# Performance work log

Measured on AMD Instinct MI355X. Metric: run time of the kernel, lower is better.

## Reference

```python
import math
import jax, jax.numpy as jnp
import numpy as np
from jax.scipy.special import xlogy, gammaln

HEADS = 8
DIM_KEY = 64
NUM_REL_POS_FEATURES = 192


def get_positional_embed(n, feature_size):
    # distances: [-n+1, ..., n-1], length 2n-1
    dist = jnp.arange(-n + 1, n)
    adist = jnp.abs(dist).astype(jnp.float32)[:, None]  # (2n-1, 1)
    num_basis = feature_size // 6  # 3 feature fns * 2 (sign-augmented)
    seq_len = n
    # exponential half-life features
    max_range = math.log(seq_len) / math.log(2.0)
    half_life = 2.0 ** jnp.linspace(3.0, max_range, num_basis)  # min_half_life=3.0
    feat_exp = jnp.exp(-math.log(2.0) / half_life[None, :] * adist)
    # central mask features
    center_widths = 2.0 ** jnp.arange(1, num_basis + 1) - 1.0
    feat_cm = (center_widths[None, :] > adist).astype(jnp.float32)
    # gamma pdf features
    stddev = seq_len / (2 * num_basis)
    start_mean = seq_len / num_basis
    mean = jnp.linspace(start_mean, float(seq_len), num_basis)[None, :]
    concentration = (mean / stddev) ** 2
    rate = mean / (stddev ** 2)
    log_unnorm = xlogy(concentration - 1.0, adist) - rate * adist
    log_norm = gammaln(concentration) - concentration * jnp.log(rate)
    prob = jnp.exp(log_unnorm - log_norm) + 1e-8
    feat_gamma = prob / jnp.max(prob, axis=-1, keepdims=True)
    emb = jnp.concatenate([feat_exp, feat_cm, feat_gamma], axis=-1)  # (2n-1, fs/2)
    sign = jnp.sign(dist).astype(jnp.float32)[:, None]
    return jnp.concatenate([emb, sign * emb], axis=-1)  # (2n-1, fs)


def relative_shift(x):
    # x: (b, h, n, 2n-1) -> (b, h, n, n) Transformer-XL shift
    b, h, t1, t2 = x.shape
    x = jnp.pad(x, ((0, 0), (0, 0), (0, 0), (1, 0)))  # (b,h,t1,t2+1)
    x = x.reshape(b, h, t2 + 1, t1)[:, :, 1:, :].reshape(b, h, t1, t2)
    return x[..., : (t2 + 2) // 2]


def setup_inputs() -> dict:
    key = jax.random.key(0)
    ks = jax.random.split(key, 8)
    dim = 1536
    b, n = 2, 1536
    hdk = HEADS * DIM_KEY  # 512
    hdv = HEADS * 192      # 1536
    s = 0.02
    return {
        'x': jax.random.normal(ks[0], (b, n, dim), jnp.float32),
        'Wq': jax.random.normal(ks[1], (hdk, dim), jnp.float32) * s,
        'Wk': jax.random.normal(ks[2], (hdk, dim), jnp.float32) * s,
        'Wv': jax.random.normal(ks[3], (hdv, dim), jnp.float32) * s,
        'Wrel': jax.random.normal(ks[4], (hdk, NUM_REL_POS_FEATURES), jnp.float32) * s,
        'Wout': jax.random.normal(ks[5], (dim, hdv), jnp.float32) * s,
        'b_out': jnp.zeros((dim,), jnp.float32),
        'rel_content_bias': jax.random.normal(ks[6], (1, HEADS, 1, DIM_KEY), jnp.float32),
        'rel_pos_bias': jax.random.normal(ks[7], (1, HEADS, 1, DIM_KEY), jnp.float32),
    }


def reference(x, Wq, Wk, Wv, Wrel, Wout, b_out, rel_content_bias, rel_pos_bias):
    b, n, dim = x.shape
    h = HEADS
    scale = DIM_KEY ** -0.5

    def split_heads(t):  # (b, n, h*d) -> (b, h, n, d)
        return t.reshape(b, n, h, -1).transpose(0, 2, 1, 3)

    q = split_heads(jnp.einsum('bnd,fd->bnf', x, Wq)) * scale
    k = split_heads(jnp.einsum('bnd,fd->bnf', x, Wk))
    v = split_heads(jnp.einsum('bnd,fd->bnf', x, Wv))

    content_logits = jnp.einsum('bhid,bhjd->bhij', q + rel_content_bias, k)

    positions = get_positional_embed(n, NUM_REL_POS_FEATURES)  # (2n-1, fs)
    rel_k = jnp.einsum('jf,ef->je', positions, Wrel).reshape(2 * n - 1, h, DIM_KEY)
    rel_k = rel_k.transpose(1, 0, 2)  # (h, 2n-1, dk)
    rel_logits = jnp.einsum('bhid,hjd->bhij', q + rel_pos_bias, rel_k)
    rel_logits = relative_shift(rel_logits)  # (b, h, n, n)

    attn = jax.nn.softmax(content_logits + rel_logits, axis=-1)
    out = jnp.einsum('bhij,bhjd->bhid', attn, v)
    out = out.transpose(0, 2, 1, 3).reshape(b, n, -1)  # (b, n, h*dv)
    return jnp.einsum('bnf,df->bnd', out, Wout) + b_out
```

## Files before the change

kernel.cpp:

```cpp
#include <hip/hip_runtime.h>
#include <cmath>

typedef unsigned short u16;
typedef unsigned int u32;
typedef short frag8 __attribute__((ext_vector_type(8)));
typedef float f32x4 __attribute__((ext_vector_type(4)));

#define DEVINL __device__ __forceinline__

DEVINL float bf2f(u16 v) { return __uint_as_float(((u32)v) << 16); }
DEVINL u16 f2bf(float f) {
    u32 u = __float_as_uint(f);
    u32 r = (u + 0x7fffu + ((u >> 16) & 1u)) >> 16;
    return (u16)r;
}
DEVINL u32 pack2(float a, float b) { return (u32)f2bf(a) | ((u32)f2bf(b) << 16); }
DEVINL void async_copy16(const u16* g, u16* l) {
    __builtin_amdgcn_global_load_lds((const __attribute__((address_space(1))) u32*)g,
                                     (__attribute__((address_space(3))) u32*)l, 16, 0, 0);
}
DEVINL f32x4 mfma_bf16(frag8 a, frag8 b, f32x4 c) {
    return __builtin_amdgcn_mfma_f32_16x16x32_bf16(a, b, c, 0, 0, 0);
}

__global__ __launch_bounds__(256) void convert_kernel(
        const float* __restrict__ s0, const float* __restrict__ s1,
        const float* __restrict__ s2, const float* __restrict__ s3,
        const float* __restrict__ s4, u16* __restrict__ dst) {
    const int c0 = 589824, c1 = 98304, c2 = 98304, c3 = 294912;
    const int total = 1376256;
    for (int c = blockIdx.x * blockDim.x + threadIdx.x; c < total;
         c += gridDim.x * blockDim.x) {
        const float* src; int off;
        if (c < c0) { src = s0; off = c; }
        else if (c < c0 + c1) { src = s1; off = c - c0; }
        else if (c < c0 + c1 + c2) { src = s2; off = c - c0 - c1; }
        else if (c < c0 + c1 + c2 + c3) { src = s3; off = c - c0 - c1 - c2; }
        else { src = s4; off = c - c0 - c1 - c2 - c3; }
        float4 a = ((const float4*)src)[off * 2];
        float4 b = ((const float4*)src)[off * 2 + 1];
        uint4 o;
        o.x = pack2(a.x, a.y); o.y = pack2(a.z, a.w);
        o.z = pack2(b.x, b.y); o.w = pack2(b.z, b.w);
        ((uint4*)dst)[c] = o;
    }
}

DEVINL double lgamma_stirling(double z) {
    double zi = 1.0 / z, zi2 = zi * zi;
    return (z - 0.5) * log(z) - z + 0.91893853320467274178
         + zi * (1.0 / 12.0) - zi * zi2 * (1.0 / 360.0) + zi * zi2 * zi2 * (1.0 / 1260.0);
}

__global__ __launch_bounds__(256) void embed_relk_kernel(const float* __restrict__ Wrel,
                                                         u16* __restrict__ relk) {
    __shared__ float pos[16][192];
    __shared__ float inv_hl[32], cwid[32], cm1[32], rateS[32];
    __shared__ double lognS[32];
    __shared__ float gmax[16];
    int t = threadIdx.x;
    int u0b = blockIdx.x * 16;

    if (t < 32) {
        double step = (10.584962500721156 - 3.0) / 31.0;
        double hl = exp2(3.0 + t * step);
        inv_hl[t] = (float)(1.0 / hl);
        cwid[t] = exp2f((float)(t + 1)) - 1.0f;
        double mean = 48.0 * (t + 1);
        double conc = (mean / 24.0) * (mean / 24.0);
        double rate = mean / 576.0;
        cm1[t] = (float)(conc - 1.0);
        rateS[t] = (float)rate;
        lognS[t] = lgamma_stirling(conc) - conc * log(rate);
    }
    __syncthreads();

    for (int idx = t; idx < 512; idx += 256) {
        int ul = idx >> 5, bs = idx & 31;
        int dist = u0b + ul - 1535;
        float ad = fabsf((float)dist);
        pos[ul][bs] = exp2f(-ad * inv_hl[bs]);
        pos[ul][32 + bs] = (cwid[bs] > ad) ? 1.0f : 0.0f;
        double prob = 0.0;
        if (dist != 0) {
            double adD = (double)ad;
            prob = exp((double)cm1[bs] * log(adD) - (double)rateS[bs] * adD - lognS[bs]);
        }
        pos[ul][64 + bs] = (float)(prob + 1e-8);
    }
    __syncthreads();
    if (t < 16) {
        float g = 0.f;
        #pragma unroll
        for (int bsx = 0; bsx < 32; bsx++) g = fmaxf(g, pos[t][64 + bsx]);
        gmax[t] = g;
    }
    __syncthreads();
    for (int idx = t; idx < 16 * 96; idx += 256) {
        int ul = idx / 96, f = idx - ul * 96;
        float v = pos[ul][f];
        if (f >= 64) { v = v / gmax[ul]; pos[ul][f] = v; }
        int dist = u0b + ul - 1535;
        float sg = (dist > 0) ? 1.f : ((dist < 0) ? -1.f : 0.f);
        pos[ul][96 + f] = sg * v;
    }
    __syncthreads();

    int e0 = t * 2;
    const float* w0 = Wrel + e0 * 192;
    const float* w1 = w0 + 192;
    float a0[16], a1[16];
    #pragma unroll
    for (int ul = 0; ul < 16; ul++) { a0[ul] = 0.f; a1[ul] = 0.f; }
    for (int f = 0; f < 192; f++) {
        float wa = w0[f], wb = w1[f];
        #pragma unroll
        for (int ul = 0; ul < 16; ul++) {
            float p = pos[ul][f];
            a0[ul] = fmaf(p, wa, a0[ul]);
            a1[ul] = fmaf(p, wb, a1[ul]);
        }
    }
    int h0 = e0 >> 6, d0 = e0 & 63;
    int h1 = (e0 + 1) >> 6, d1 = (e0 + 1) & 63;
    for (int ul = 0; ul < 16; ul++) {
        int u = u0b + ul;
        relk[(h0 * 3072 + u) * 64 + d0] = f2bf(a0[ul]);
        relk[(h1 * 3072 + u) * 64 + d1] = f2bf(a1[ul]);
    }
}

DEVINL void gemm128_mainloop(const u16* __restrict__ A, const u16* __restrict__ B,
                             int K, f32x4 acc[4][4], u16* As, u16* Bs) {
    int tid = threadIdx.x;
    int lane = tid & 63, wave = tid >> 6;
    int wm = (wave >> 1) * 64, wn = (wave & 1) * 64;
    int fm = lane & 15, fq = lane >> 4;
    for (int k0 = 0; k0 < K; k0 += 32) {
        #pragma unroll
        for (int p = 0; p < 2; p++) {
            int e = (p * 256 + tid) * 8;
            int r = e >> 5, c = e & 31;
            async_copy16(A + r * K + k0 + c, As + e);
            async_copy16(B + r * K + k0 + c, Bs + e);
        }
        __syncthreads();
        frag8 af[4], bfr[4];
        #pragma unroll
        for (int mi = 0; mi < 4; mi++) af[mi] = *(const frag8*)&As[(wm + 16 * mi + fm) * 32 + fq * 8];
        #pragma unroll
        for (int ni = 0; ni < 4; ni++) bfr[ni] = *(const frag8*)&Bs[(wn + 16 * ni + fm) * 32 + fq * 8];
        #pragma unroll
        for (int mi = 0; mi < 4; mi++)
            #pragma unroll
            for (int ni = 0; ni < 4; ni++)
                acc[mi][ni] = mfma_bf16(af[mi], bfr[ni], acc[mi][ni]);
        __syncthreads();
    }
}

__global__ __launch_bounds__(256) void gemm_qkv_kernel(
        const u16* __restrict__ X, const u16* __restrict__ Wq, const u16* __restrict__ Wk,
        const u16* __restrict__ Wv, const float* __restrict__ cbias, const float* __restrict__ pbias,
        u16* __restrict__ qc, u16* __restrict__ qp, u16* __restrict__ kws, u16* __restrict__ vt) {
    __shared__ __align__(16) u16 As[128 * 32];
    __shared__ __align__(16) u16 Bs[128 * 32];
    int m0 = blockIdx.x * 128, n0 = blockIdx.y * 128;
    const u16* Bp; int brow;
    if (n0 < 512)       { Bp = Wq; brow = n0; }
    else if (n0 < 1024) { Bp = Wk; brow = n0 - 512; }
    else                { Bp = Wv; brow = n0 - 1024; }
    f32x4 acc[4][4];
    #pragma unroll
    for (int i = 0; i < 4; i++)
        #pragma unroll
        for (int j = 0; j < 4; j++) acc[i][j] = (f32x4){0.f, 0.f, 0.f, 0.f};
    gemm128_mainloop(X + m0 * 1536, Bp + brow * 1536, 1536, acc, As, Bs);

    int tid = threadIdx.x, lane = tid & 63, wave = tid >> 6;
    int wm = (wave >> 1) * 64, wn = (wave & 1) * 64, fm = lane & 15, fq = lane >> 4;
    #pragma unroll
    for (int mi = 0; mi < 4; mi++) {
        #pragma unroll
        for (int ni = 0; ni < 4; ni++) {
            int col = n0 + wn + 16 * ni + fm;
            int rbase = m0 + wm + 16 * mi + fq * 4;
            #pragma unroll
            for (int reg = 0; reg < 4; reg++) {
                int row = rbase + reg;
                float v = acc[mi][ni][reg];
                int b = row >= 1536 ? 1 : 0;
                int i = row - b * 1536;
                if (n0 < 512) {
                    float qv = v * 0.125f;
                    int idx = ((b * 8 + (col >> 6)) * 1536 + i) * 64 + (col & 63);
                    qc[idx] = f2bf(qv + cbias[col]);
                    qp[idx] = f2bf(qv + pbias[col]);
                } else if (n0 < 1024) {
                    int c2 = col - 512;
                    kws[((b * 8 + (c2 >> 6)) * 1536 + i) * 64 + (c2 & 63)] = f2bf(v);
                } else {
                    int c2 = col - 1024;
                    int hh = c2 / 192, dd = c2 - hh * 192;
                    vt[((b * 8 + hh) * 192 + dd) * 1536 + i] = f2bf(v);
                }
            }
        }
    }
}

#define SP 68
#define RP 100

__global__ __launch_bounds__(256, 3) void attn_kernel(
        const u16* __restrict__ qc, const u16* __restrict__ qp, const u16* __restrict__ kws,
        const u16* __restrict__ vt, const u16* __restrict__ relk, u16* __restrict__ ao) {
    __shared__ __align__(16) float S_lds[32 * SP];
    __shared__ __align__(16) float R_lds[32 * RP];
    __shared__ __align__(16) u16 P_lds[32 * 64];
    __shared__ float mstate[32], lstate[32], alpha_lds[32];

    const int n = 1536;
    int bh = blockIdx.y, b = bh >> 3, h = bh & 7;
    int i0 = blockIdx.x * 32;
    const u16* qcP = qc + bh * n * 64;
    const u16* qpP = qp + bh * n * 64;

    int tid = threadIdx.x, lane = tid & 63, w = tid >> 6, fm = lane & 15, fq = lane >> 4;
    int sw = fm & 7;
    if (tid < 32) { mstate[tid] = __int_as_float(0xff800000); lstate[tid] = 0.f; }

    frag8 aqc[2][2], aqp[2][2];
    #pragma unroll
    for (int mi = 0; mi < 2; mi++)
        #pragma unroll
        for (int ks = 0; ks < 2; ks++) {
            int off = (i0 + 16 * mi + fm) * 64 + ks * 32 + fq * 8;
            aqc[mi][ks] = *(const frag8*)(qcP + off);
            aqp[mi][ks] = *(const frag8*)(qpP + off);
        }

    f32x4 acc_o[2][3];
    #pragma unroll
    for (int mi = 0; mi < 2; mi++)
        #pragma unroll
        for (int dj = 0; dj < 3; dj++) acc_o[mi][dj] = (f32x4){0.f, 0.f, 0.f, 0.f};

    int uis[3], rmis[3];
    #pragma unroll
    for (int tt = 0; tt < 3; tt++) {
        int tv = w + tt * 4;
        rmis[tt] = (tv >= 6) ? 1 : 0;
        uis[tt] = tv - rmis[tt] * 6;
    }

    const u16* kIt  = kws + bh * n * 64 + (16 * w + fm) * 64 + fq * 8;
    const u16* vIt  = vt + bh * 192 * n + (48 * w + fm) * 1536 + fq * 8;
    const u16* rk0  = relk + h * 3072 * 64 + (1504 - i0 + fm) * 64 + fq * 8 + uis[0] * 1024;
    const u16* rk1  = relk + h * 3072 * 64 + (1504 - i0 + fm) * 64 + fq * 8 + uis[1] * 1024;
    const u16* rk2  = relk + h * 3072 * 64 + (1504 - i0 + fm) * 64 + fq * 8 + uis[2] * 1024;

    for (int jt = 0; jt < 24; jt++) {
        frag8 fk[2], fr0[2], fr1[2], fr2[2];
        fk[0]  = *(const frag8*)(kIt);
        fk[1]  = *(const frag8*)(kIt + 32);
        fr0[0] = *(const frag8*)(rk0);
        fr0[1] = *(const frag8*)(rk0 + 32);
        fr1[0] = *(const frag8*)(rk1);
        fr1[1] = *(const frag8*)(rk1 + 32);
        fr2[0] = *(const frag8*)(rk2);
        fr2[1] = *(const frag8*)(rk2 + 32);
        kIt += 4096; rk0 += 4096; rk1 += 4096; rk2 += 4096;

        f32x4 acc_s[2];
        acc_s[0] = (f32x4){0.f, 0.f, 0.f, 0.f};
        acc_s[1] = (f32x4){0.f, 0.f, 0.f, 0.f};
        #pragma unroll
        for (int ks = 0; ks < 2; ks++) {
            acc_s[0] = mfma_bf16(aqc[0][ks], fk[ks], acc_s[0]);
            acc_s[1] = mfma_bf16(aqc[1][ks], fk[ks], acc_s[1]);
        }
        f32x4 acc_r[3];
        #pragma unroll
        for (int tt = 0; tt < 3; tt++) acc_r[tt] = (f32x4){0.f, 0.f, 0.f, 0.f};
        #pragma unroll
        for (int ks = 0; ks < 2; ks++) {
            acc_r[0] = mfma_bf16(aqp[rmis[0]][ks], fr0[ks], acc_r[0]);
            acc_r[1] = mfma_bf16(aqp[rmis[1]][ks], fr1[ks], acc_r[1]);
            acc_r[2] = mfma_bf16(aqp[rmis[2]][ks], fr2[ks], acc_r[2]);
        }

        #pragma unroll
        for (int mi = 0; mi < 2; mi++)
            #pragma unroll
            for (int reg = 0; reg < 4; reg++)
                S_lds[(16 * mi + fq * 4 + reg) * SP + 16 * w + fm] = acc_s[mi][reg];
        #pragma unroll
        for (int tt = 0; tt < 3; tt++)
            #pragma unroll
            for (int reg = 0; reg < 4; reg++)
                R_lds[(16 * rmis[tt] + fq * 4 + reg) * RP + 16 * uis[tt] + fm] = acc_r[tt][reg];
        __syncthreads();

        frag8 fv[3][2];
        #pragma unroll
        for (int dj = 0; dj < 3; dj++)
            #pragma unroll
            for (int ks = 0; ks < 2; ks++)
                fv[dj][ks] = *(const frag8*)(vIt + dj * 24576 + ks * 32);
        vIt += 64;

        int li = tid >> 3, c0 = (tid & 7) * 8;
        float sv[8];
        {
            float4 sa = *(const float4*)(S_lds + li * SP + c0);
            float4 sb = *(const float4*)(S_lds + li * SP + c0 + 4);
            sv[0] = sa.x; sv[1] = sa.y; sv[2] = sa.z; sv[3] = sa.w;
            sv[4] = sb.x; sv[5] = sb.y; sv[6] = sb.z; sv[7] = sb.w;
        }
        const float* rrow = R_lds + li * RP + c0 - li + 31;
        float mx = __int_as_float(0xff800000);
        #pragma unroll
        for (int e = 0; e < 8; e++) {
            sv[e] += rrow[e];
            mx = fmaxf(mx, sv[e]);
        }
        mx = fmaxf(mx, __shfl_xor(mx, 1));
        mx = fmaxf(mx, __shfl_xor(mx, 2));
        mx = fmaxf(mx, __shfl_xor(mx, 4));
        float mo = mstate[li];
        float mn = fmaxf(mo, mx);
        float al = __expf(mo - mn);
        float pe[8], sum = 0.f;
        #pragma unroll
        for (int e = 0; e < 8; e++) { pe[e] = __expf(sv[e] - mn); sum += pe[e]; }
        {
            uint4 pw;
            pw.x = pack2(pe[0], pe[1]); pw.y = pack2(pe[2], pe[3]);
            pw.z = pack2(pe[4], pe[5]); pw.w = pack2(pe[6], pe[7]);
            int slot = (tid & 7) ^ (li & 7);
            *(uint4*)&P_lds[li * 64 + slot * 8] = pw;
        }
        sum += __shfl_xor(sum, 1);
        sum += __shfl_xor(sum, 2);
        sum += __shfl_xor(sum, 4);
        if ((tid & 7) == 0) {
            mstate[li] = mn;
            lstate[li] = lstate[li] * al + sum;
            alpha_lds[li] = al;
        }
        __syncthreads();

        #pragma unroll
        for (int mi = 0; mi < 2; mi++)
            #pragma unroll
            for (int reg = 0; reg < 4; reg++) {
                float al2 = alpha_lds[16 * mi + fq * 4 + reg];
                #pragma unroll
                for (int dj = 0; dj < 3; dj++) acc_o[mi][dj][reg] *= al2;
            }
        frag8 ap[2][2];
        #pragma unroll
        for (int mi = 0; mi < 2; mi++)
            #pragma unroll
            for (int ks = 0; ks < 2; ks++)
                ap[mi][ks] = *(const frag8*)&P_lds[(16 * mi + fm) * 64 + ((ks * 4 + fq) ^ sw) * 8];
        #pragma unroll
        for (int dj = 0; dj < 3; dj++) {
            #pragma unroll
            for (int ks = 0; ks < 2; ks++) {
                acc_o[0][dj] = mfma_bf16(ap[0][ks], fv[dj][ks], acc_o[0][dj]);
                acc_o[1][dj] = mfma_bf16(ap[1][ks], fv[dj][ks], acc_o[1][dj]);
            }
        }
    }

    #pragma unroll
    for (int mi = 0; mi < 2; mi++)
        #pragma unroll
        for (int dj = 0; dj < 3; dj++)
            #pragma unroll
            for (int reg = 0; reg < 4; reg++) {
                int rl = 16 * mi + fq * 4 + reg;
                float lsum = lstate[rl];
                int row = b * 1536 + i0 + rl;
                int col = h * 192 + 16 * (3 * w + dj) + fm;
                ao[row * 1536 + col] = f2bf(acc_o[mi][dj][reg] / lsum);
            }
}

__global__ __launch_bounds__(256) void gemm_out_kernel(
        const u16* __restrict__ A, const u16* __restrict__ W, const float* __restrict__ bias,
        float* __restrict__ out) {
    __shared__ __align__(16) u16 As[128 * 32];
    __shared__ __align__(16) u16 Bs[128 * 32];
    int m0 = blockIdx.x * 128, n0 = blockIdx.y * 128;
    f32x4 acc[4][4];
    #pragma unroll
    for (int i = 0; i < 4; i++)
        #pragma unroll
        for (int j = 0; j < 4; j++) acc[i][j] = (f32x4){0.f, 0.f, 0.f, 0.f};
    gemm128_mainloop(A + m0 * 1536, W + n0 * 1536, 1536, acc, As, Bs);

    int tid = threadIdx.x, lane = tid & 63, wave = tid >> 6;
    int wm = (wave >> 1) * 64, wn = (wave & 1) * 64, fm = lane & 15, fq = lane >> 4;
    #pragma unroll
    for (int mi = 0; mi < 4; mi++) {
        #pragma unroll
        for (int ni = 0; ni < 4; ni++) {
            int col = n0 + wn + 16 * ni + fm;
            int rbase = m0 + wm + 16 * mi + fq * 4;
            float bv = bias[col];
            #pragma unroll
            for (int reg = 0; reg < 4; reg++) {
                int row = rbase + reg;
                out[row * 1536 + col] = acc[mi][ni][reg] + bv;
            }
        }
    }
}

extern "C" void kernel_launch(void* const* d_in, const int* in_sizes, int n_in,
                              void* d_out, int out_size, void* d_ws, size_t ws_size,
                              hipStream_t stream) {
    (void)in_sizes; (void)n_in; (void)out_size; (void)ws_size;
    const float* x    = (const float*)d_in[0];
    const float* Wq   = (const float*)d_in[1];
    const float* Wk   = (const float*)d_in[2];
    const float* Wv   = (const float*)d_in[3];
    const float* Wrel = (const float*)d_in[4];
    const float* Wout = (const float*)d_in[5];
    const float* bout = (const float*)d_in[6];
    const float* cb   = (const float*)d_in[7];
    const float* pb   = (const float*)d_in[8];

    u16* xb  = (u16*)d_ws;
    u16* wqb = xb  + 4718592;
    u16* wkb = wqb + 786432;
    u16* wvb = wkb + 786432;
    u16* wob = wvb + 2359296;
    u16* qc  = wob + 2359296;
    u16* qp  = qc + 1572864;
    u16* kw  = qp + 1572864;
    u16* vt  = kw + 1572864;
    u16* rk  = vt + 4718592;
    u16* ao  = rk + 1572864;
    float* out = (float*)d_out;

    convert_kernel<<<dim3(1024), dim3(256), 0, stream>>>(x, Wq, Wk, Wv, Wout, xb);
    embed_relk_kernel<<<dim3(192), dim3(256), 0, stream>>>(Wrel, rk);
    gemm_qkv_kernel<<<dim3(24, 20), dim3(256), 0, stream>>>(xb, wqb, wkb, wvb, cb, pb, qc, qp, kw, vt);
    attn_kernel<<<dim3(48, 16), dim3(256), 0, stream>>>(qc, qp, kw, vt, rk, ao);
    gemm_out_kernel<<<dim3(24, 12), dim3(256), 0, stream>>>(ao, wob, bout, out);
}
```

Baseline: 343.8 us.

## Prefetch next K/relK fragments, use lighter barriers, and swizzle block order

Loads for the next iteration's K and rel-K fragments are issued right after the current MFMAs, so global latency overlaps the softmax and PV work. __syncthreads is replaced with a barrier that waits only on LDS counters, letting outstanding global loads stay in flight across the barrier. Block indices are remapped so consecutive blocks go to different heads or batches, which changes how K and V are shared in cache. The costs are extra registers for the prefetched fragments, which may reduce occupancy, and reliance on LDS-only waits being sufficient for correctness.

```diff
diff --git a/kernel.cpp b/kernel.cpp
--- a/kernel.cpp
+++ b/kernel.cpp
@@ -21,6 +21,11 @@
 }
 DEVINL f32x4 mfma_bf16(frag8 a, frag8 b, f32x4 c) {
     return __builtin_amdgcn_mfma_f32_16x16x32_bf16(a, b, c, 0, 0, 0);
+}
+DEVINL void bar_sync() {
+    asm volatile("s_waitcnt lgkmcnt(0)" ::: "memory");
+    __builtin_amdgcn_s_barrier();
+    asm volatile("" ::: "memory");
 }
 
 __global__ __launch_bounds__(256) void convert_kernel(
@@ -221,8 +226,11 @@
     __shared__ float mstate[32], lstate[32], alpha_lds[32];
 
     const int n = 1536;
-    int bh = blockIdx.y, b = bh >> 3, h = bh & 7;
-    int i0 = blockIdx.x * 32;
+    int flat = blockIdx.y * 48 + blockIdx.x;
+    int swz  = (flat & 7) * 96 + (flat >> 3);
+    int bh = swz / 48;
+    int i0 = (swz - bh * 48) * 32;
+    int b = bh >> 3, h = bh & 7;
     const u16* qcP = qc + bh * n * 64;
     const u16* qpP = qp + bh * n * 64;
 
@@ -254,24 +262,25 @@
         uis[tt] = tv - rmis[tt] * 6;
     }
 
-    const u16* kIt  = kws + bh * n * 64 + (16 * w + fm) * 64 + fq * 8;
-    const u16* vIt  = vt + bh * 192 * n + (48 * w + fm) * 1536 + fq * 8;
-    const u16* rk0  = relk + h * 3072 * 64 + (1504 - i0 + fm) * 64 + fq * 8 + uis[0] * 1024;
-    const u16* rk1  = relk + h * 3072 * 64 + (1504 - i0 + fm) * 64 + fq * 8 + uis[1] * 1024;
-    const u16* rk2  = relk + h * 3072 * 64 + (1504 - i0 + fm) * 64 + fq * 8 + uis[2] * 1024;
+    const u16* kIt = kws + bh * n * 64 + (16 * w + fm) * 64 + fq * 8;
+    const u16* vIt = vt + bh * 192 * n + (48 * w + fm) * 1536 + fq * 8;
+    const u16* rkp[3];
+    #pragma unroll
+    for (int tt = 0; tt < 3; tt++)
+        rkp[tt] = relk + h * 3072 * 64 + (1504 - i0 + fm) * 64 + fq * 8 + uis[tt] * 1024;
+
+    frag8 fk[2], fr[3][2];
+    fk[0] = *(const frag8*)(kIt);
+    fk[1] = *(const frag8*)(kIt + 32);
+    #pragma unroll
+    for (int tt = 0; tt < 3; tt++) {
+        fr[tt][0] = *(const frag8*)(rkp[tt]);
+        fr[tt][1] = *(const frag8*)(rkp[tt] + 32);
+    }
+    kIt += 4096;
+    rkp[0] += 4096; rkp[1] += 4096; rkp[2] += 4096;
 
     for (int jt = 0; jt < 24; jt++) {
-        frag8 fk[2], fr0[2], fr1[2], fr2[2];
-        fk[0]  = *(const frag8*)(kIt);
-        fk[1]  = *(const frag8*)(kIt + 32);
-        fr0[0] = *(const frag8*)(rk0);
-        fr0[1] = *(const frag8*)(rk0 + 32);
-        fr1[0] = *(const frag8*)(rk1);
-        fr1[1] = *(const frag8*)(rk1 + 32);
-        fr2[0] = *(const frag8*)(rk2);
-        fr2[1] = *(const frag8*)(rk2 + 32);
-        kIt += 4096; rk0 += 4096; rk1 += 4096; rk2 += 4096;
-
         f32x4 acc_s[2];
         acc_s[0] = (f32x4){0.f, 0.f, 0.f, 0.f};
         acc_s[1] = (f32x4){0.f, 0.f, 0.f, 0.f};
@@ -285,9 +294,21 @@
         for (int tt = 0; tt < 3; tt++) acc_r[tt] = (f32x4){0.f, 0.f, 0.f, 0.f};
         #pragma unroll
         for (int ks = 0; ks < 2; ks++) {
-            acc_r[0] = mfma_bf16(aqp[rmis[0]][ks], fr0[ks], acc_r[0]);
-            acc_r[1] = mfma_bf16(aqp[rmis[1]][ks], fr1[ks], acc_r[1]);
-            acc_r[2] = mfma_bf16(aqp[rmis[2]][ks], fr2[ks], acc_r[2]);
+            acc_r[0] = mfma_bf16(aqp[rmis[0]][ks], fr[0][ks], acc_r[0]);
+            acc_r[1] = mfma_bf16(aqp[rmis[1]][ks], fr[1][ks], acc_r[1]);
+            acc_r[2] = mfma_bf16(aqp[rmis[2]][ks], fr[2][ks], acc_r[2]);
+        }
+
+        if (jt < 23) {
+            fk[0] = *(const frag8*)(kIt);
+            fk[1] = *(const frag8*)(kIt + 32);
+            #pragma unroll
+            for (int tt = 0; tt < 3; tt++) {
+                fr[tt][0] = *(const frag8*)(rkp[tt]);
+                fr[tt][1] = *(const frag8*)(rkp[tt] + 32);
+            }
+            kIt += 4096;
+            rkp[0] += 4096; rkp[1] += 4096; rkp[2] += 4096;
         }
 
         #pragma unroll
@@ -300,7 +321,7 @@
             #pragma unroll
             for (int reg = 0; reg < 4; reg++)
                 R_lds[(16 * rmis[tt] + fq * 4 + reg) * RP + 16 * uis[tt] + fm] = acc_r[tt][reg];
-        __syncthreads();
+        bar_sync();
 
         frag8 fv[3][2];
         #pragma unroll
@@ -349,7 +370,7 @@
             lstate[li] = lstate[li] * al + sum;
             alpha_lds[li] = al;
         }
-        __syncthreads();
+        bar_sync();
 
         #pragma unroll
         for (int mi = 0; mi < 2; mi++)
```

Result: slower. 359.5 us (+4.6%).
